# Optimization experiments

Hardware: AMD Instinct MI355X
Metric: run time of the kernel (lower is better)

The kernel has to match this reference:

```python
import jax, jax.numpy as jnp
import numpy as np

EPS = 1e-12
WA = 0.002


def _radial_bins(h: int, w: int):
    """Static (numpy) replication of torch _radial_masks: centered integer radial
    bins, then fftshift'd (matching the original code exactly)."""
    y = np.linspace(-(h // 2), h // 2 - (1 if h % 2 == 0 else 0), h)
    x = np.linspace(-(w // 2), w // 2 - (1 if w % 2 == 0 else 0), w)
    yy, xx = np.meshgrid(y, x, indexing='ij')
    dist = np.sqrt(xx ** 2 + yy ** 2)
    max_bin = int(dist.max())  # torch: int(max) then clamp -> no-op since dist>=0
    bins = np.clip(dist.astype(np.int32), 0, max_bin)
    bins = np.fft.fftshift(bins)
    return jnp.asarray(bins.reshape(-1)), max_bin


def setup_inputs() -> dict:
    key = jax.random.key(0)
    B, H, W = 16, 1024, 1024
    prob_cg = jax.random.uniform(key, (B, 1, H, W), dtype=jnp.float32)
    return {"prob_cg": prob_cg}


def reference(prob_cg) -> jnp.ndarray:
    B, C, H, W = prob_cg.shape
    seg, max_bin = _radial_bins(H, W)  # [H*W] int32 bin ids, static max_bin
    n_bins = max_bin + 1

    # Power spectrum P(f) = |fftshift(fft2(p))|^2 / N.
    # (torch code fftshifts all dims incl. batch; that is a pure batch permutation
    #  and the final loss is a mean over batch, so shifting only spatial axes is
    #  mathematically identical.)
    p = prob_cg[:, 0].astype(jnp.float32)
    fv = jnp.fft.fftshift(jnp.fft.fft2(p, axes=(-2, -1)), axes=(-2, -1))
    power = (fv.real ** 2 + fv.imag ** 2) / (H * W)  # [B,H,W]

    # Radial segment-mean over integer-radius annuli (replaces the O(B*R*H*W)
    # double loop with a single O(B*H*W) scatter-add).
    flat = power.reshape(B, H * W)
    sums = jax.vmap(lambda v: jax.ops.segment_sum(v, seg, num_segments=n_bins))(flat)
    counts = jax.ops.segment_sum(jnp.ones((H * W,), jnp.float32), seg, num_segments=n_bins)
    radial = jnp.where(counts > 0, sums / jnp.maximum(counts, 1.0), 0.0)  # [B,n_bins]

    # Broadcast radial mean back to the grid and accumulate squared deviation.
    radial_expanded = radial[:, seg].reshape(B, H, W)
    loss = jnp.mean(jnp.sum((power - radial_expanded + EPS) ** 2, axis=(-2, -1)))
    return WA * loss
```

## Files before the change

### kernel.cpp

```cpp
#include <hip/hip_runtime.h>
#include <math.h>

#define NB 16
#define NPAIR 8
#define NBINS 725
#define NPIX (1024*1024)

#define SLOT(idx, c) ((idx)*9 + (c) + ((idx)>>5))
#define SH_SIZE 9248

__device__ __forceinline__ constexpr int rev5(int j) {
    return ((j&1)<<4) | ((j&2)<<2) | (j&4) | ((j&8)>>2) | ((j&16)>>4);
}

__device__ __forceinline__ void fft32(float2* r) {
    const float wr[16] = {1.f, 0.98078528f, 0.92387953f, 0.83146961f,
                          0.70710678f, 0.55557023f, 0.38268343f, 0.19509032f,
                          0.f, -0.19509032f, -0.38268343f, -0.55557023f,
                          -0.70710678f, -0.83146961f, -0.92387953f, -0.98078528f};
    const float wi[16] = {0.f, -0.19509032f, -0.38268343f, -0.55557023f,
                          -0.70710678f, -0.83146961f, -0.92387953f, -0.98078528f,
                          -1.f, -0.98078528f, -0.92387953f, -0.83146961f,
                          -0.70710678f, -0.55557023f, -0.38268343f, -0.19509032f};
    #pragma unroll
    for (int s = 1; s <= 5; ++s) {
        const int half = 1 << (s - 1);
        #pragma unroll
        for (int g = 0; g < 32; g += (1 << s)) {
            #pragma unroll
            for (int j = 0; j < half; ++j) {
                const float cw = wr[j << (5 - s)], sw = wi[j << (5 - s)];
                int i1 = g + j, i2 = i1 + half;
                float2 u = r[i1], v = r[i2];
                float2 vw = make_float2(v.x * cw - v.y * sw, v.x * sw + v.y * cw);
                r[i1] = make_float2(u.x + vw.x, u.y + vw.y);
                r[i2] = make_float2(u.x - vw.x, u.y - vw.y);
            }
        }
    }
}

__device__ __forceinline__ void twiddle1024(float2* r, int n1) {
    float sn, cs;
    sincosf((float)n1 * -0.006135923151542565f, &sn, &cs);
    float wx = 1.f, wy = 0.f;
    #pragma unroll
    for (int k2 = 0; k2 < 32; ++k2) {
        float2 s = r[k2];
        r[k2] = make_float2(s.x * wx - s.y * wy, s.x * wy + s.y * wx);
        float nx = wx * cs - wy * sn;
        wy = wx * sn + wy * cs;
        wx = nx;
    }
}

__device__ __forceinline__ int ibin(int d2) {
    int bin = (int)sqrtf((float)d2);
    if ((bin + 1) * (bin + 1) <= d2) ++bin;
    else if (bin * bin > d2) --bin;
    return bin;
}

__device__ __forceinline__ int col_of(int k, int c) {
    if (k == 0) return (c < 4) ? c : ((c == 4) ? 512 : 1028 - c);
    int a = k << 2;
    return (c < 4) ? (a + c) : (1017 + c - a);
}
__device__ __forceinline__ int mir_of(int k, int c) {
    if (k == 0) return (c == 0 || c == 4) ? c : ((c < 4) ? c + 4 : c - 4);
    return 7 - c;
}

__global__ __launch_bounds__(256, 2) void fft_rows(const float* __restrict__ in,
                                                   float2* __restrict__ spec,
                                                   float* __restrict__ cntp) {
    __shared__ float2 sh[SH_SIZE];
    __shared__ float hc[NBINS];
    int tid = threadIdx.x, blk = blockIdx.x;
    int p = blk >> 7, y0 = (blk & 127) << 3;
    if (p == 0)
        for (int i = tid; i < NBINS; i += 256) hc[i] = 0.f;
    int n1 = tid & 31, c = tid >> 5;
    const float* xr = in + (((size_t)(2 * p)) << 20) + ((size_t)(y0 + c) << 10);
    const float* yr = xr + (1u << 20);
    float2 r[32];
    #pragma unroll
    for (int j = 0; j < 32; ++j) {
        int n = n1 + (rev5(j) << 5);
        r[j] = make_float2(xr[n], yr[n]);
    }
    fft32(r);
    twiddle1024(r, n1);
    int sb = 9 * n1 + c;
    #pragma unroll
    for (int k2 = 0; k2 < 32; ++k2) sh[sb + 289 * k2] = r[k2];
    __syncthreads();
    int k2 = tid & 31;
    int rb = 289 * k2 + c;
    #pragma unroll
    for (int j = 0; j < 32; ++j) r[j] = sh[rb + 9 * rev5(j)];
    fft32(r);
    __syncthreads();
    int wb = 9 * k2 + c;
    #pragma unroll
    for (int k1 = 0; k1 < 32; ++k1) sh[wb + 289 * k1] = r[k1];
    __syncthreads();
    float2* base = spec + (((size_t)p) << 20);
    for (int rep = 0; rep < 32; ++rep) {
        int idx = (rep << 8) + tid;
        int kcol = idx >> 3, cc = idx & 7;
        base[((size_t)kcol << 10) + y0 + cc] = sh[SLOT(kcol, cc)];
    }
    if (p == 0) {
        int g = blk;
        int row = (g << 2) + (tid >> 6);
        int xb = (tid & 63) << 4;
        int dy = row - 512, dy2 = dy * dy;
        int curbin = -1;
        float a = 0.f;
        #pragma unroll 4
        for (int j = 0; j < 16; ++j) {
            int x = xb + j;
            float w = 2.f;
            if (row == 0) w = (x > 512 || x == 0) ? 0.f : ((x == 512) ? 1.f : 2.f);
            int dx = x - 512;
            int bin = ibin(dy2 + dx * dx);
            if (bin == curbin) a += w;
            else {
                if (curbin >= 0 && a != 0.f) atomicAdd(&hc[curbin], a);
                curbin = bin; a = w;
            }
        }
        if (curbin >= 0 && a != 0.f) atomicAdd(&hc[curbin], a);
        if (g == 0) {
            int xb2 = tid << 2;
            int curb = -1;
            float aa = 0.f;
            #pragma unroll
            for (int j = 0; j < 4; ++j) {
                int xx = xb2 + j;
                if (xx > 512) continue;
                float w = ((xx & 511) == 0) ? 1.f : 2.f;
                int bin = 512 - xx;
                if (bin == curb) aa += w;
                else {
                    if (curb >= 0 && aa != 0.f) atomicAdd(&hc[curb], aa);
                    curb = bin; aa = w;
                }
            }
            if (curb >= 0 && aa != 0.f) atomicAdd(&hc[curb], aa);
        }
        __syncthreads();
        for (int i = tid; i < NBINS; i += 256)
            cntp[(size_t)g * NBINS + i] = hc[i];
    }
}

__global__ __launch_bounds__(256, 2) void fft_cols_hist(const float2* __restrict__ spec,
                                                        float* __restrict__ s2buf,
                                                        float* __restrict__ partial) {
    __shared__ float2 sh[SH_SIZE];
    __shared__ float hs0[NBINS], hs1[NBINS];
    __shared__ float wred[8];
    int tid = threadIdx.x, blk = blockIdx.x;
    int p = blk >> 7, k = blk & 127;
    for (int i = tid; i < NBINS; i += 256) { hs0[i] = 0.f; hs1[i] = 0.f; }
    int n1 = tid & 31, c = tid >> 5;
    const float2* base = spec + (((size_t)p) << 20);
    const float2* colp = base + ((size_t)col_of(k, c) << 10);
    float2 r[32];
    #pragma unroll
    for (int j = 0; j < 32; ++j) r[j] = colp[n1 + (rev5(j) << 5)];
    fft32(r);
    twiddle1024(r, n1);
    int sb = 9 * n1 + c;
    #pragma unroll
    for (int q = 0; q < 32; ++q) sh[sb + 289 * q] = r[q];
    __syncthreads();
    int k2 = tid & 31;
    int rb = 289 * k2 + c;
    #pragma unroll
    for (int j = 0; j < 32; ++j) r[j] = sh[rb + 9 * rev5(j)];
    __syncthreads();
    fft32(r);
    int wb = 9 * k2 + c;
    #pragma unroll
    for (int k1 = 0; k1 < 32; ++k1) sh[wb + 289 * k1] = r[k1];
    __syncthreads();
    const float inv = 1.0f / (float)NPIX;
    int cl = tid & 7, chunk = tid >> 3;
    int xcol = col_of(k, cl), mc = mir_of(k, cl);
    int dxv = xcol - 512, dx2 = dxv * dxv;
    bool xs = ((xcol & 511) == 0), xhi = (xcol > 512);
    float s2e = 0.f, s2o = 0.f;
    int curbin = -1;
    float a0 = 0.f, a1 = 0.f;
    int ky0 = chunk << 4;
    #pragma unroll 4
    for (int j = 0; j < 16; ++j) {
        int ky = ky0 + j;
        float w = 2.f;
        if (ky == 0) w = xhi ? 0.f : ((xcol == 0) ? 0.f : (xs ? 1.f : 2.f));
        int my = (1024 - ky) & 1023;
        float2 f1 = sh[SLOT(ky, cl)];
        float2 f2 = sh[SLOT(my, mc)];
        float xr = 0.5f * (f1.x + f2.x), xi = 0.5f * (f1.y - f2.y);
        float yr = 0.5f * (f1.y + f2.y), yi = 0.5f * (f2.x - f1.x);
        float pe = (xr * xr + xi * xi) * inv;
        float po = (yr * yr + yi * yi) * inv;
        int dy = ky - 512;
        int bin = ibin(dy * dy + dx2);
        float v0 = w * pe, v1 = w * po;
        s2e += v0 * pe;
        s2o += v1 * po;
        if (bin == curbin) { a0 += v0; a1 += v1; }
        else {
            if (curbin >= 0) { atomicAdd(&hs0[curbin], a0); atomicAdd(&hs1[curbin], a1); }
            curbin = bin; a0 = v0; a1 = v1;
        }
    }
    if (curbin >= 0) { atomicAdd(&hs0[curbin], a0); atomicAdd(&hs1[curbin], a1); }
    if (tid < 8) {
        int x2 = col_of(k, tid);
        if (x2 <= 512) {
            int mc2 = mir_of(k, tid);
            float w = ((x2 & 511) == 0) ? 1.f : 2.f;
            float2 f1 = sh[SLOT(512, tid)];
            float2 f2 = sh[SLOT(512, mc2)];
            float xr = 0.5f * (f1.x + f2.x), xi = 0.5f * (f1.y - f2.y);
            float yr = 0.5f * (f1.y + f2.y), yi = 0.5f * (f2.x - f1.x);
            float pe = (xr * xr + xi * xi) * inv;
            float po = (yr * yr + yi * yi) * inv;
            float v0 = w * pe, v1 = w * po;
            s2e += v0 * pe;
            s2o += v1 * po;
            int bin = (x2 < 512) ? 512 - x2 : 0;
            atomicAdd(&hs0[bin], v0);
            atomicAdd(&hs1[bin], v1);
        }
    }
    #pragma unroll
    for (int off = 32; off > 0; off >>= 1) {
        s2e += __shfl_down(s2e, off);
        s2o += __shfl_down(s2o, off);
    }
    if ((tid & 63) == 0) { wred[tid >> 6] = s2e; wred[4 + (tid >> 6)] = s2o; }
    __syncthreads();
    if (tid == 0) s2buf[2 * blk]     = wred[0] + wred[1] + wred[2] + wred[3];
    if (tid == 1) s2buf[2 * blk + 1] = wred[4] + wred[5] + wred[6] + wred[7];
    float* pe = partial + ((size_t)(2 * p) * 128 + k) * NBINS;
    float* po = partial + ((size_t)(2 * p + 1) * 128 + k) * NBINS;
    for (int i = tid; i < NBINS; i += 256) {
        pe[i] = hs0[i];
        po[i] = hs1[i];
    }
}

__global__ __launch_bounds__(256) void reduce_loss(const float* __restrict__ partial,
                                                   const float* __restrict__ cntp,
                                                   float* __restrict__ rowval) {
    int b = blockIdx.x / 3, band = blockIdx.x % 3;
    int bin = band * 256 + threadIdx.x;
    if (bin >= NBINS) return;
    const float* bp = partial + (size_t)b * 128 * NBINS + bin;
    float s = 0.f;
    #pragma unroll 8
    for (int k = 0; k < 128; ++k) s += bp[(size_t)k * NBINS];
    float cv = 0.f;
    #pragma unroll 8
    for (int g = 0; g < 128; ++g) cv += cntp[(size_t)g * NBINS + bin];
    rowval[b * NBINS + bin] = (cv > 0.f) ? s * s / cv : 0.f;
}

__global__ __launch_bounds__(256) void final_out(const float* __restrict__ s2buf,
                                                 const float* __restrict__ rowval,
                                                 float* __restrict__ out) {
    __shared__ float red[256];
    int tid = threadIdx.x;
    float acc = 0.f;
    for (int i = tid; i < NB * NBINS; i += 256) acc -= rowval[i];
    for (int i = tid; i < 2 * NPAIR * 128; i += 256) acc += s2buf[i];
    red[tid] = acc;
    __syncthreads();
    for (int s = 128; s > 0; s >>= 1) {
        if (tid < s) red[tid] += red[tid + s];
        __syncthreads();
    }
    if (tid == 0) out[0] = red[0] * (0.002f / 16.0f);
}

extern "C" void kernel_launch(void* const* d_in, const int* in_sizes, int n_in,
                              void* d_out, int out_size, void* d_ws, size_t ws_size,
                              hipStream_t stream) {
    const float* in = (const float*)d_in[0];
    float* out = (float*)d_out;
    char* ws = (char*)d_ws;

    float2* spec   = (float2*)ws;
    float* s2buf   = (float*)(ws + ((size_t)NPAIR << 20) * sizeof(float2));
    float* rowval  = s2buf + 2 * NPAIR * 128;
    float* cntp    = rowval + NB * NBINS;
    float* partial = cntp + 128 * NBINS;

    fft_rows<<<NPAIR * 128, 256, 0, stream>>>(in, spec, cntp);
    fft_cols_hist<<<NPAIR * 128, 256, 0, stream>>>(spec, s2buf, partial);
    reduce_loss<<<NB * 3, 256, 0, stream>>>(partial, cntp, rowval);
    final_out<<<1, 256, 0, stream>>>(s2buf, rowval, out);
}
```

Baseline: 117.1 us.

## Store FFT intermediates as packed bf16 complex in global and shared memory

```diff
diff --git a/kernel.cpp b/kernel.cpp
--- a/kernel.cpp
+++ b/kernel.cpp
@@ -8,6 +8,17 @@
 
 #define SLOT(idx, c) ((idx)*9 + (c) + ((idx)>>5))
 #define SH_SIZE 9248
+
+__device__ __forceinline__ unsigned bf16rn(float f) {
+    unsigned u = __float_as_uint(f);
+    return (u + 0x7FFFu + ((u >> 16) & 1u)) >> 16;
+}
+__device__ __forceinline__ unsigned pk2(float2 v) {
+    return bf16rn(v.x) | (bf16rn(v.y) << 16);
+}
+__device__ __forceinline__ float2 up2(unsigned v) {
+    return make_float2(__uint_as_float(v << 16), __uint_as_float(v & 0xFFFF0000u));
+}
 
 __device__ __forceinline__ constexpr int rev5(int j) {
     return ((j&1)<<4) | ((j&2)<<2) | (j&4) | ((j&8)>>2) | ((j&16)>>4);
@@ -71,10 +82,10 @@
     return 7 - c;
 }
 
-__global__ __launch_bounds__(256, 2) void fft_rows(const float* __restrict__ in,
-                                                   float2* __restrict__ spec,
+__global__ __launch_bounds__(256, 4) void fft_rows(const float* __restrict__ in,
+                                                   unsigned* __restrict__ spec,
                                                    float* __restrict__ cntp) {
-    __shared__ float2 sh[SH_SIZE];
+    __shared__ unsigned sh[SH_SIZE];
     __shared__ float hc[NBINS];
     int tid = threadIdx.x, blk = blockIdx.x;
     int p = blk >> 7, y0 = (blk & 127) << 3;
@@ -93,19 +104,19 @@
     twiddle1024(r, n1);
     int sb = 9 * n1 + c;
     #pragma unroll
-    for (int k2 = 0; k2 < 32; ++k2) sh[sb + 289 * k2] = r[k2];
+    for (int k2 = 0; k2 < 32; ++k2) sh[sb + 289 * k2] = pk2(r[k2]);
     __syncthreads();
     int k2 = tid & 31;
     int rb = 289 * k2 + c;
     #pragma unroll
-    for (int j = 0; j < 32; ++j) r[j] = sh[rb + 9 * rev5(j)];
+    for (int j = 0; j < 32; ++j) r[j] = up2(sh[rb + 9 * rev5(j)]);
     fft32(r);
     __syncthreads();
     int wb = 9 * k2 + c;
     #pragma unroll
-    for (int k1 = 0; k1 < 32; ++k1) sh[wb + 289 * k1] = r[k1];
-    __syncthreads();
-    float2* base = spec + (((size_t)p) << 20);
+    for (int k1 = 0; k1 < 32; ++k1) sh[wb + 289 * k1] = pk2(r[k1]);
+    __syncthreads();
+    unsigned* base = spec + (((size_t)p) << 20);
     for (int rep = 0; rep < 32; ++rep) {
         int idx = (rep << 8) + tid;
         int kcol = idx >> 3, cc = idx & 7;
@@ -156,39 +167,39 @@
     }
 }
 
-__global__ __launch_bounds__(256, 2) void fft_cols_hist(const float2* __restrict__ spec,
+__global__ __launch_bounds__(256, 3) void fft_cols_hist(const unsigned* __restrict__ spec,
                                                         float* __restrict__ s2buf,
                                                         float* __restrict__ partial) {
-    __shared__ float2 sh[SH_SIZE];
+    __shared__ unsigned sh[SH_SIZE];
     __shared__ float hs0[NBINS], hs1[NBINS];
     __shared__ float wred[8];
     int tid = threadIdx.x, blk = blockIdx.x;
     int p = blk >> 7, k = blk & 127;
     for (int i = tid; i < NBINS; i += 256) { hs0[i] = 0.f; hs1[i] = 0.f; }
     int n1 = tid & 31, c = tid >> 5;
-    const float2* base = spec + (((size_t)p) << 20);
-    const float2* colp = base + ((size_t)col_of(k, c) << 10);
+    const unsigned* base = spec + (((size_t)p) << 20);
+    const unsigned* colp = base + ((size_t)col_of(k, c) << 10);
     float2 r[32];
     #pragma unroll
-    for (int j = 0; j < 32; ++j) r[j] = colp[n1 + (rev5(j) << 5)];
+    for (int j = 0; j < 32; ++j) r[j] = up2(colp[n1 + (rev5(j) << 5)]);
     fft32(r);
     twiddle1024(r, n1);
     int sb = 9 * n1 + c;
     #pragma unroll
-    for (int q = 0; q < 32; ++q) sh[sb + 289 * q] = r[q];
+    for (int q = 0; q < 32; ++q) sh[sb + 289 * q] = pk2(r[q]);
     __syncthreads();
     int k2 = tid & 31;
     int rb = 289 * k2 + c;
     #pragma unroll
-    for (int j = 0; j < 32; ++j) r[j] = sh[rb + 9 * rev5(j)];
+    for (int j = 0; j < 32; ++j) r[j] = up2(sh[rb + 9 * rev5(j)]);
     __syncthreads();
     fft32(r);
     int wb = 9 * k2 + c;
     #pragma unroll
-    for (int k1 = 0; k1 < 32; ++k1) sh[wb + 289 * k1] = r[k1];
+    for (int k1 = 0; k1 < 32; ++k1) sh[wb + 289 * k1] = pk2(r[k1]);
     __syncthreads();
     const float inv = 1.0f / (float)NPIX;
-    int cl = tid & 7, chunk = tid >> 3;
+    int cl = tid >> 5, chunk = tid & 31;
     int xcol = col_of(k, cl), mc = mir_of(k, cl);
     int dxv = xcol - 512, dx2 = dxv * dxv;
     bool xs = ((xcol & 511) == 0), xhi = (xcol > 512);
@@ -202,8 +213,8 @@
         float w = 2.f;
         if (ky == 0) w = xhi ? 0.f : ((xcol == 0) ? 0.f : (xs ? 1.f : 2.f));
         int my = (1024 - ky) & 1023;
-        float2 f1 = sh[SLOT(ky, cl)];
-        float2 f2 = sh[SLOT(my, mc)];
+        float2 f1 = up2(sh[SLOT(ky, cl)]);
+        float2 f2 = up2(sh[SLOT(my, mc)]);
         float xr = 0.5f * (f1.x + f2.x), xi = 0.5f * (f1.y - f2.y);
         float yr = 0.5f * (f1.y + f2.y), yi = 0.5f * (f2.x - f1.x);
         float pe = (xr * xr + xi * xi) * inv;
@@ -220,13 +231,14 @@
         }
     }
     if (curbin >= 0) { atomicAdd(&hs0[curbin], a0); atomicAdd(&hs1[curbin], a1); }
-    if (tid < 8) {
-        int x2 = col_of(k, tid);
+    if ((tid & 31) == 0) {
+        int cl2 = tid >> 5;
+        int x2 = col_of(k, cl2);
         if (x2 <= 512) {
-            int mc2 = mir_of(k, tid);
+            int mc2 = mir_of(k, cl2);
             float w = ((x2 & 511) == 0) ? 1.f : 2.f;
-            float2 f1 = sh[SLOT(512, tid)];
-            float2 f2 = sh[SLOT(512, mc2)];
+            float2 f1 = up2(sh[SLOT(512, cl2)]);
+            float2 f2 = up2(sh[SLOT(512, mc2)]);
             float xr = 0.5f * (f1.x + f2.x), xi = 0.5f * (f1.y - f2.y);
             float yr = 0.5f * (f1.y + f2.y), yi = 0.5f * (f2.x - f1.x);
             float pe = (xr * xr + xi * xi) * inv;
@@ -296,8 +308,8 @@
     float* out = (float*)d_out;
     char* ws = (char*)d_ws;
 
-    float2* spec   = (float2*)ws;
-    float* s2buf   = (float*)(ws + ((size_t)NPAIR << 20) * sizeof(float2));
+    unsigned* spec = (unsigned*)ws;
+    float* s2buf   = (float*)(ws + ((size_t)NPAIR << 20) * sizeof(unsigned));
     float* rowval  = s2buf + 2 * NPAIR * 128;
     float* cntp    = rowval + NB * NBINS;
     float* partial = cntp + 128 * NBINS;
```

Result: faster. 103.5 us (-11.6%).
